# Optimization experiments

Measured on AMD Instinct MI355X. Metric: run time of the kernel, lower is better.

The kernel has to match this reference:

```python
import jax, jax.numpy as jnp
import numpy as np

N_FREQ = 256
VOCAB = 50257
N_CHANNELS = 1024
B, S = 4, 1024


def setup_inputs() -> dict:
    key = jax.random.key(0)
    k1, k2 = jax.random.split(key)
    h = jax.random.normal(k1, (B, S, N_CHANNELS), dtype=jnp.float32)
    weight = jax.random.normal(k2, (N_CHANNELS, 2 * N_FREQ), dtype=jnp.float32) * 0.02
    return {"h": h, "weight": weight}


def reference(h, weight):
    n = N_FREQ
    V = VOCAB
    # channel -> frequency coefficients (real part then imag part)
    Y_ri = h.astype(jnp.float32) @ weight  # [B, S, 2n]
    Y = jax.lax.complex(Y_ri[..., :n], Y_ri[..., n:])  # [B, S, n]
    # zero-padded half-spectrum: bins 1..n carry Y, DC and high bins are zero
    full = jnp.zeros(h.shape[:-1] + (V // 2 + 1,), dtype=jnp.complex64)
    full = full.at[..., 1:n + 1].set(Y)
    out = jnp.fft.irfft(full, n=V, axis=-1)  # [B, S, V]
    return out.astype(h.dtype)
```

## Files before the change

kernel.cpp:

```cpp
#include <hip/hip_runtime.h>
#include <hip/hip_fp16.h>
#include <stdint.h>

#define V_N   50257
#define NPAN  393
#define NCH   1024
#define MT    4096
#define KC    512
#define NFRQ  256
#define TWO_PI 6.28318530717958647692f

typedef _Float16 f16;
typedef __attribute__((ext_vector_type(8))) _Float16 f16x8;
typedef __attribute__((ext_vector_type(4))) float    f32x4;

#define CFENCE asm volatile("" ::: "memory")

__global__ __launch_bounds__(256) void k1_proj(
    const float* __restrict__ h, const float* __restrict__ w, f16* __restrict__ A) {
  __shared__ __align__(16) f16 As[64 * 64];
  __shared__ __align__(16) f16 Bs[64 * 64];
  const int tid = threadIdx.x;
  const int bn0 = blockIdx.x * 64;
  const int bm0 = blockIdx.y * 64;
  const int lane = tid & 63, wid = tid >> 6;
  const int lr = lane & 15, lg = lane >> 4;
  const int wr = wid >> 1, wc = wid & 1;

  f32x4 acc[2][2];
#pragma unroll
  for (int i = 0; i < 2; ++i)
#pragma unroll
    for (int j = 0; j < 2; ++j) acc[i][j] = (f32x4){0.f, 0.f, 0.f, 0.f};

  for (int s = 0; s < NCH / 64; ++s) {
    const int k0 = s * 64;
    __syncthreads();
#pragma unroll
    for (int r = 0; r < 2; ++r) {
      int q = tid + r * 256;
      int m = q >> 3, c = q & 7;
      const float* src = h + (size_t)(bm0 + m) * NCH + k0 + c * 8;
      f32x4 v0 = *(const f32x4*)src;
      f32x4 v1 = *(const f32x4*)(src + 4);
      f16x8 pk;
#pragma unroll
      for (int e = 0; e < 4; ++e) { pk[e] = (f16)v0[e]; pk[4 + e] = (f16)v1[e]; }
      *(f16x8*)&As[m * 64 + ((c ^ (m & 7)) << 3)] = pk;
    }
#pragma unroll
    for (int r = 0; r < 2; ++r) {
      int q = tid + r * 256;
      int c = q >> 6, n = q & 63;
      int jj = bn0 + n;
      int wcol = (jj >> 1) + ((jj & 1) ? NFRQ : 0);
      f16x8 pk;
#pragma unroll
      for (int j = 0; j < 8; ++j)
        pk[j] = (f16)w[(size_t)(k0 + c * 8 + j) * KC + wcol];
      *(f16x8*)&Bs[n * 64 + ((c ^ (n & 7)) << 3)] = pk;
    }
    __syncthreads();
#pragma unroll
    for (int kk = 0; kk < 2; ++kk) {
      const int cb = kk * 4 + lg;
      f16x8 a[2], b[2];
#pragma unroll
      for (int mi = 0; mi < 2; ++mi) {
        int row = wr * 32 + mi * 16 + lr;
        a[mi] = *(const f16x8*)&As[row * 64 + ((cb ^ (row & 7)) << 3)];
      }
#pragma unroll
      for (int ni = 0; ni < 2; ++ni) {
        int col = wc * 32 + ni * 16 + lr;
        b[ni] = *(const f16x8*)&Bs[col * 64 + ((cb ^ (col & 7)) << 3)];
      }
#pragma unroll
      for (int mi = 0; mi < 2; ++mi)
#pragma unroll
        for (int ni = 0; ni < 2; ++ni)
          acc[mi][ni] = __builtin_amdgcn_mfma_f32_16x16x32_f16(a[mi], b[ni], acc[mi][ni], 0, 0, 0);
    }
  }
#pragma unroll
  for (int mi = 0; mi < 2; ++mi)
#pragma unroll
    for (int ni = 0; ni < 2; ++ni)
#pragma unroll
      for (int r = 0; r < 4; ++r) {
        int row = bm0 + wr * 32 + mi * 16 + lg * 4 + r;
        int col = bn0 + wc * 32 + ni * 16 + lr;
        int r16 = row >> 4, lrA = row & 15;
        int kt = col >> 6, q = col & 63;
        int ks = q >> 5, lgA = (q >> 3) & 3, e = q & 7;
        size_t off = ((((size_t)r16 * 8 + kt) * 2 + ks) * 4 + lgA) * 128 + lrA * 8 + e;
        A[off] = (f16)acc[mi][ni][r];
      }
}


__device__ __forceinline__ void load_a(const f16* __restrict__ A, int bm0, int wr,
                                       int kt, int lane, f16x8 a[4][2]) {
  const int r16b = (bm0 >> 4) + wr * 4;
#pragma unroll
  for (int mi = 0; mi < 4; ++mi)
#pragma unroll
    for (int ks = 0; ks < 2; ++ks) {
      size_t off = (((size_t)(r16b + mi) * 8 + kt) * 2 + ks) * 512 + (size_t)lane * 8;
      a[mi][ks] = *(const f16x8*)&A[off];
    }
}

__device__ __forceinline__ void compute_reg(
    const f16x8 a[4][2], const f16* __restrict__ CB,
    int wr, int wc, int lr, int lg, f32x4 acc[4][4]) {
#pragma unroll
  for (int ks = 0; ks < 2; ++ks) {
    const int cb = ks * 4 + lg;
    f16x8 b[4];
#pragma unroll
    for (int ni = 0; ni < 4; ++ni) {
      int col = wc * 64 + ni * 16 + lr;
      b[ni] = *(const f16x8*)&CB[col * 64 + ((cb ^ (col & 7)) << 3)];
    }
    __builtin_amdgcn_s_setprio(1);
#pragma unroll
    for (int mi = 0; mi < 4; ++mi)
#pragma unroll
      for (int ni = 0; ni < 4; ++ni)
        acc[mi][ni] = __builtin_amdgcn_mfma_f32_16x16x32_f16(a[mi][ks], b[ni], acc[mi][ni], 0, 0, 0);
    __builtin_amdgcn_s_setprio(0);
  }
}

__device__ __forceinline__ void seed_base(int s, int g, int t, float& br, float& bi) {
  int fb = 32 * s + 16 * g;
  int m = (fb * t) % V_N;
  float sn, cs;
  __sincosf((TWO_PI / (float)V_N) * (float)m, &sn, &cs);
  br = cs; bi = sn;
}

__device__ __forceinline__ void gen_bt(const float Tr[16], const float Ti[16],
                                       float br, float bi, f16x8 bt[4]) {
#pragma unroll
  for (int u = 0; u < 4; ++u)
#pragma unroll
    for (int p = 0; p < 4; ++p) {
      const int j = 4 * u + p;
      float re = br * Tr[j] - bi * Ti[j];
      float im = br * Ti[j] + bi * Tr[j];
      bt[u][2 * p]     = (f16)re;
      bt[u][2 * p + 1] = (f16)(-im);
    }
}

__device__ __forceinline__ void store_bt(f16* Bs, int nloc, int g, const f16x8 bt[4]) {
#pragma unroll
  for (int u = 0; u < 4; ++u) {
    int c = 4 * g + u;
    *(f16x8*)&Bs[nloc * 64 + ((c ^ (nloc & 7)) << 3)] = bt[u];
  }
}

#define K2_TILE(S, AC, AN)                                                \
  do {                                                                    \
    enum { s_ = (S) };                                                    \
    if (s_ < 7) {                                                         \
      load_a(A, bm0, wr, s_ + 1, lane, AN);                               \
      float br_, bi_;                                                     \
      seed_base(s_ + 1, g, t, br_, bi_);                                  \
      gen_bt(Tr, Ti, br_, bi_, btn);                                      \
    }                                                                     \
    CFENCE;                                                               \
    asm volatile("s_waitcnt lgkmcnt(0)" ::: "memory");                    \
    __builtin_amdgcn_s_barrier();                                         \
    compute_reg(AC, Bs, wr, wc, lr, lg, acc);                             \
    CFENCE;                                                               \
    __builtin_amdgcn_s_barrier();                                         \
    if (s_ < 7) store_bt(Bs, nloc, g, btn);                               \
  } while (0)

__global__ __launch_bounds__(256, 2) void k2_areg(
    const f16* __restrict__ A, float* __restrict__ out) {
  __shared__ __align__(16) f16 Bs[128 * 64];
  const int tid = threadIdx.x;
  const int orig = blockIdx.x;
  const int wgid = (orig & 7) * 1572 + (orig >> 3);
  const int by = wgid / 393;
  const int bx = wgid - by * 393;
  const int bn0 = bx << 7;
  const int bm0 = by << 7;
  const int lane = tid & 63, wid = tid >> 6;
  const int lr = lane & 15, lg = lane >> 4;
  const int wr = wid >> 1, wc = wid & 1;

  const int nloc = tid & 127;
  const int g = tid >> 7;
  int t = bn0 + nloc;
  if (t >= V_N) t -= V_N;
  const float w0 = TWO_PI / (float)V_N;
  float Tr[16], Ti[16];
#pragma unroll
  for (int j = 0; j < 16; ++j) {
    int m = ((j + 1) * t) % V_N;
    float sn, cs;
    __sincosf(w0 * (float)m, &sn, &cs);
    Tr[j] = cs; Ti[j] = sn;
  }

  f32x4 acc[4][4];
#pragma unroll
  for (int i = 0; i < 4; ++i)
#pragma unroll
    for (int j = 0; j < 4; ++j) acc[i][j] = (f32x4){0.f, 0.f, 0.f, 0.f};

  {
    float br, bi;
    seed_base(0, g, t, br, bi);
    f16x8 bt[4];
    gen_bt(Tr, Ti, br, bi, bt);
    store_bt(Bs, nloc, g, bt);
  }
  f16x8 aA[4][2], aB[4][2], btn[4];
  load_a(A, bm0, wr, 0, lane, aA);

  K2_TILE(0, aA, aB);
  K2_TILE(1, aB, aA);
  K2_TILE(2, aA, aB);
  K2_TILE(3, aB, aA);
  K2_TILE(4, aA, aB);
  K2_TILE(5, aB, aA);
  K2_TILE(6, aA, aB);
  K2_TILE(7, aB, aA);

  const float scale = 2.0f / (float)V_N;
#pragma unroll
  for (int ni = 0; ni < 4; ++ni) {
    int col = bn0 + wc * 64 + ni * 16 + lr;
    if (col < V_N) {
#pragma unroll
      for (int mi = 0; mi < 4; ++mi)
#pragma unroll
        for (int r = 0; r < 4; ++r) {
          int row = bm0 + wr * 64 + mi * 16 + lg * 4 + r;
          out[(size_t)row * V_N + col] = acc[mi][ni][r] * scale;
        }
    }
  }
}

extern "C" void kernel_launch(void* const* d_in, const int* in_sizes, int n_in,
                              void* d_out, int out_size, void* d_ws, size_t ws_size,
                              hipStream_t stream) {
  const float* h = (const float*)d_in[0];
  const float* w = (const float*)d_in[1];
  float* out = (float*)d_out;
  f16* A = (f16*)d_ws;

  dim3 blk(256);
  hipLaunchKernelGGL(k1_proj, dim3(KC / 64, MT / 64), blk, 0, stream, h, w, A);
  hipLaunchKernelGGL(k2_areg, dim3(NPAN * 32), blk, 0, stream, A, out);
}
```

Measured before the change: 386.4 us.

## Generate twiddle B fragments directly in registers, dropping LDS and barriers

```diff
diff --git a/kernel.cpp b/kernel.cpp
--- a/kernel.cpp
+++ b/kernel.cpp
@@ -13,8 +13,6 @@
 typedef _Float16 f16;
 typedef __attribute__((ext_vector_type(8))) _Float16 f16x8;
 typedef __attribute__((ext_vector_type(4))) float    f32x4;
-
-#define CFENCE asm volatile("" ::: "memory")
 
 __global__ __launch_bounds__(256) void k1_proj(
     const float* __restrict__ h, const float* __restrict__ w, f16* __restrict__ A) {
@@ -111,79 +109,39 @@
     }
 }
 
-__device__ __forceinline__ void compute_reg(
-    const f16x8 a[4][2], const f16* __restrict__ CB,
-    int wr, int wc, int lr, int lg, f32x4 acc[4][4]) {
-#pragma unroll
-  for (int ks = 0; ks < 2; ++ks) {
-    const int cb = ks * 4 + lg;
-    f16x8 b[4];
-#pragma unroll
-    for (int ni = 0; ni < 4; ++ni) {
-      int col = wc * 64 + ni * 16 + lr;
-      b[ni] = *(const f16x8*)&CB[col * 64 + ((cb ^ (col & 7)) << 3)];
-    }
-    __builtin_amdgcn_s_setprio(1);
-#pragma unroll
-    for (int mi = 0; mi < 4; ++mi)
-#pragma unroll
-      for (int ni = 0; ni < 4; ++ni)
-        acc[mi][ni] = __builtin_amdgcn_mfma_f32_16x16x32_f16(a[mi][ks], b[ni], acc[mi][ni], 0, 0, 0);
-    __builtin_amdgcn_s_setprio(0);
-  }
-}
-
-__device__ __forceinline__ void seed_base(int s, int g, int t, float& br, float& bi) {
-  int fb = 32 * s + 16 * g;
-  int m = (fb * t) % V_N;
-  float sn, cs;
-  __sincosf((TWO_PI / (float)V_N) * (float)m, &sn, &cs);
-  br = cs; bi = sn;
-}
-
-__device__ __forceinline__ void gen_bt(const float Tr[16], const float Ti[16],
-                                       float br, float bi, f16x8 bt[4]) {
-#pragma unroll
-  for (int u = 0; u < 4; ++u)
-#pragma unroll
-    for (int p = 0; p < 4; ++p) {
-      const int j = 4 * u + p;
-      float re = br * Tr[j] - bi * Ti[j];
-      float im = br * Ti[j] + bi * Tr[j];
-      bt[u][2 * p]     = (f16)re;
-      bt[u][2 * p + 1] = (f16)(-im);
-    }
-}
-
-__device__ __forceinline__ void store_bt(f16* Bs, int nloc, int g, const f16x8 bt[4]) {
-#pragma unroll
-  for (int u = 0; u < 4; ++u) {
-    int c = 4 * g + u;
-    *(f16x8*)&Bs[nloc * 64 + ((c ^ (nloc & 7)) << 3)] = bt[u];
-  }
-}
-
-#define K2_TILE(S, AC, AN)                                                \
-  do {                                                                    \
-    enum { s_ = (S) };                                                    \
-    if (s_ < 7) {                                                         \
-      load_a(A, bm0, wr, s_ + 1, lane, AN);                               \
-      float br_, bi_;                                                     \
-      seed_base(s_ + 1, g, t, br_, bi_);                                  \
-      gen_bt(Tr, Ti, br_, bi_, btn);                                      \
-    }                                                                     \
-    CFENCE;                                                               \
-    asm volatile("s_waitcnt lgkmcnt(0)" ::: "memory");                    \
-    __builtin_amdgcn_s_barrier();                                         \
-    compute_reg(AC, Bs, wr, wc, lr, lg, acc);                             \
-    CFENCE;                                                               \
-    __builtin_amdgcn_s_barrier();                                         \
-    if (s_ < 7) store_bt(Bs, nloc, g, btn);                               \
+#define K2_TILE(S, AC, AN)                                                     \
+  do {                                                                         \
+    enum { s_ = (S) };                                                         \
+    if (s_ < 7) load_a(A, bm0, wr, s_ + 1, lane, AN);                          \
+    _Pragma("unroll") for (int ks = 0; ks < 2; ++ks) {                         \
+      f16x8 b[4];                                                              \
+      _Pragma("unroll") for (int ni = 0; ni < 4; ++ni) {                       \
+        const int f0 = s_ * 32 + ks * 16 + lg * 4 + 1;                         \
+        int m_ = (f0 * tn[ni]) % V_N;                                          \
+        float sb, cb2;                                                         \
+        __sincosf(w0 * (float)m_, &sb, &cb2);                                  \
+        float r1 = cb2 * T1r[ni] - sb * T1i[ni];                               \
+        float i1 = cb2 * T1i[ni] + sb * T1r[ni];                               \
+        float r2 = cb2 * T2r[ni] - sb * T2i[ni];                               \
+        float i2 = cb2 * T2i[ni] + sb * T2r[ni];                               \
+        float r3 = cb2 * T3r[ni] - sb * T3i[ni];                               \
+        float i3 = cb2 * T3i[ni] + sb * T3r[ni];                               \
+        b[ni][0] = (f16)cb2; b[ni][1] = (f16)(-sb);                            \
+        b[ni][2] = (f16)r1;  b[ni][3] = (f16)(-i1);                            \
+        b[ni][4] = (f16)r2;  b[ni][5] = (f16)(-i2);                            \
+        b[ni][6] = (f16)r3;  b[ni][7] = (f16)(-i3);                            \
+      }                                                                        \
+      __builtin_amdgcn_s_setprio(1);                                           \
+      _Pragma("unroll") for (int mi = 0; mi < 4; ++mi)                         \
+      _Pragma("unroll") for (int ni = 0; ni < 4; ++ni)                         \
+        acc[mi][ni] = __builtin_amdgcn_mfma_f32_16x16x32_f16(                  \
+            (AC)[mi][ks], b[ni], acc[mi][ni], 0, 0, 0);                        \
+      __builtin_amdgcn_s_setprio(0);                                           \
+    }                                                                          \
   } while (0)
 
-__global__ __launch_bounds__(256, 2) void k2_areg(
+__global__ __launch_bounds__(256, 2) void k2_pure(
     const f16* __restrict__ A, float* __restrict__ out) {
-  __shared__ __align__(16) f16 Bs[128 * 64];
   const int tid = threadIdx.x;
   const int orig = blockIdx.x;
   const int wgid = (orig & 7) * 1572 + (orig >> 3);
@@ -195,18 +153,21 @@
   const int lr = lane & 15, lg = lane >> 4;
   const int wr = wid >> 1, wc = wid & 1;
 
-  const int nloc = tid & 127;
-  const int g = tid >> 7;
-  int t = bn0 + nloc;
-  if (t >= V_N) t -= V_N;
   const float w0 = TWO_PI / (float)V_N;
-  float Tr[16], Ti[16];
-#pragma unroll
-  for (int j = 0; j < 16; ++j) {
-    int m = ((j + 1) * t) % V_N;
-    float sn, cs;
-    __sincosf(w0 * (float)m, &sn, &cs);
-    Tr[j] = cs; Ti[j] = sn;
+  int tn[4];
+  float T1r[4], T1i[4], T2r[4], T2i[4], T3r[4], T3i[4];
+#pragma unroll
+  for (int ni = 0; ni < 4; ++ni) {
+    int t = bn0 + wc * 64 + ni * 16 + lr;
+    if (t >= V_N) t -= V_N;
+    tn[ni] = t;
+    float s1, c1, s2, c2, s3, c3;
+    __sincosf(w0 * (float)t, &s1, &c1);
+    __sincosf(w0 * (float)((2 * t) % V_N), &s2, &c2);
+    __sincosf(w0 * (float)((3 * t) % V_N), &s3, &c3);
+    T1r[ni] = c1; T1i[ni] = s1;
+    T2r[ni] = c2; T2i[ni] = s2;
+    T3r[ni] = c3; T3i[ni] = s3;
   }
 
   f32x4 acc[4][4];
@@ -215,14 +176,7 @@
 #pragma unroll
     for (int j = 0; j < 4; ++j) acc[i][j] = (f32x4){0.f, 0.f, 0.f, 0.f};
 
-  {
-    float br, bi;
-    seed_base(0, g, t, br, bi);
-    f16x8 bt[4];
-    gen_bt(Tr, Ti, br, bi, bt);
-    store_bt(Bs, nloc, g, bt);
-  }
-  f16x8 aA[4][2], aB[4][2], btn[4];
+  f16x8 aA[4][2], aB[4][2];
   load_a(A, bm0, wr, 0, lane, aA);
 
   K2_TILE(0, aA, aB);
@@ -260,5 +214,5 @@
 
   dim3 blk(256);
   hipLaunchKernelGGL(k1_proj, dim3(KC / 64, MT / 64), blk, 0, stream, h, w, A);
-  hipLaunchKernelGGL(k2_areg, dim3(NPAN * 32), blk, 0, stream, A, out);
-}
+  hipLaunchKernelGGL(k2_pure, dim3(NPAN * 32), blk, 0, stream, A, out);
+}
```

After: 428.6 us. 10.9% more time.
